# Optimization experiments

Hardware: AMD Instinct MI355X
Metric: run time of the kernel (lower is better)

Reference implementation:

```python
import jax, jax.numpy as jnp
import numpy as np

B, S, H, D = 1, 8192, 16, 128
BS = 64            # sparse_block_size
NB = S // BS       # 128 blocks
NUM_ORACLES = 32
ORACLE = S // NUM_ORACLES          # 256
LOCAL = ORACLE // BS               # 4 sliding-window blocks
PATTERN_ID = 0


def _build_block_pattern():
    """Block-level mask exactly as DKernelPredefinedSparseAttention.create_mask((0,))."""
    qb = np.arange(NB)[:, None]
    kb = np.arange(NB)[None, :]
    causal = qb >= kb
    window = (qb - kb) < LOCAL
    vert = np.zeros(NB, dtype=bool)
    real_col = int(PATTERN_ID * ORACLE + 0.5)
    vert[real_col // BS:(real_col + ORACLE) // BS] = True
    vert[0:1] = True
    mask = causal & (window | vert[None, :])
    kmax = int(mask.sum(axis=1).max())  # = 8 for this pattern
    kidx = np.zeros((NB, kmax), dtype=np.int32)
    kvalid = np.zeros((NB, kmax), dtype=bool)
    for i in range(NB):
        idx = np.nonzero(mask[i])[0]
        kidx[i, :len(idx)] = idx
        kvalid[i, :len(idx)] = True
    return kidx, kvalid


def setup_inputs() -> dict:
    key = jax.random.key(0)
    kq, kk, kv = jax.random.split(key, 3)
    q = jax.random.normal(kq, (B, S, H, D), dtype=jnp.float32)
    k = jax.random.normal(kk, (B, S, H, D), dtype=jnp.float32)
    v = jax.random.normal(kv, (B, S, H, D), dtype=jnp.float32)
    kidx_np, kvalid_np = _build_block_pattern()
    return {"q": q, "k": k, "v": v,
            "kidx": jnp.asarray(kidx_np), "kvalid": jnp.asarray(kvalid_np)}


def reference(q, k, v, kidx, kvalid):
    # q,k,v: [B,S,H,D] (bshd). kidx/kvalid: [NB, Kmax] active k-block ids per q-block.
    b, s, h, d = q.shape
    nb = s // BS
    kmax = kidx.shape[1]
    qb = q.reshape(b, nb, BS, h, d)
    kb = k.reshape(b, nb, BS, h, d)
    vb = v.reshape(b, nb, BS, h, d)
    # Gather only active k/v blocks -> [B, nb, Kmax, BS, H, D]
    kg = kb[:, kidx]
    vg = vb[:, kidx]
    scale = 1.0 / jnp.sqrt(jnp.float32(d))
    # [B, H, nb, BS(q), Kmax, BS(k)]
    scores = jnp.einsum('bqahd,bqkchd->bhqakc', qb, kg) * scale
    # element-level causal mask within the block pattern
    qpos = jnp.arange(nb)[:, None] * BS + jnp.arange(BS)[None, :]          # [nb, BS]
    kpos = kidx[..., None] * BS + jnp.arange(BS)[None, None, :]            # [nb, Kmax, BS]
    allow = (qpos[:, :, None, None] >= kpos[:, None, :, :]) & kvalid[:, None, :, None]
    scores = jnp.where(allow[None, None], scores, jnp.float32(-1e30))
    probs = jax.nn.softmax(scores.reshape(b, h, nb, BS, kmax * BS), axis=-1)
    probs = probs.reshape(scores.shape)
    out = jnp.einsum('bhqakc,bqkchd->bqahd', probs, vg)
    return out.reshape(b, s, h, d)
```

## Files before the change

kernel.cpp:

```cpp
#include <hip/hip_runtime.h>
#include <hip/hip_bf16.h>

#define HH 16
#define DD 128
#define NBQ 128
#define SS 8192

typedef __attribute__((ext_vector_type(4))) float f32x4;
typedef __attribute__((ext_vector_type(4))) short bf16x4;
typedef __attribute__((ext_vector_type(8))) short bf16x8;

__device__ __forceinline__ short f2bf_hw(float f) {
  __hip_bfloat16 b = __float2bfloat16(f);
  return __builtin_bit_cast(short, b);
}

__device__ __forceinline__ void gload_lds16(const void* g, void* l) {
  __builtin_amdgcn_global_load_lds(
      (const __attribute__((address_space(1))) void*)g,
      (__attribute__((address_space(3))) void*)l, 16, 0, 0);
}

__device__ __forceinline__ void wg_barrier() {
  asm volatile("" ::: "memory");
  __builtin_amdgcn_s_barrier();
  asm volatile("" ::: "memory");
}

__global__ __launch_bounds__(256)
void conv_fused_kernel(const float* __restrict__ kg, const float* __restrict__ vg,
                       unsigned short* __restrict__ kt2, unsigned short* __restrict__ vt3) {
  __shared__ __align__(16) unsigned short tile[128 * 72];
  const int bx  = blockIdx.x;
  const int tid = threadIdx.x;
  if (bx < 2048) {
    const int kb = bx & 127, h = bx >> 7;
    {
      const int r = tid >> 2, q = tid & 3;
      const float* vp = vg + ((size_t)(kb * 64 + r) * HH + h) * DD + q * 32;
      #pragma unroll
      for (int c = 0; c < 8; ++c) {
        f32x4 a = *(const f32x4*)(vp + c * 4);
        #pragma unroll
        for (int j = 0; j < 4; ++j)
          tile[(q * 32 + c * 4 + j) * 72 + r] = (unsigned short)f2bf_hw(a[j]);
      }
    }
    __syncthreads();
    char* obase = (char*)vt3 + (((size_t)h * NBQ + kb) << 14);
    const int l15 = tid & 15, lg = (tid >> 4) & 3;
    #pragma unroll
    for (int round = 0; round < 4; ++round) {
      const int o  = round * 4096 + tid * 16;
      const int u  = round * 4 + (tid >> 6);
      const int nd = u >> 1, hb = u & 1;
      const int d  = nd * 16 + l15;
      bf16x8 f;
      #pragma unroll
      for (int j = 0; j < 8; ++j) {
        const int key = (2 * hb + (j >> 2)) * 16 + lg * 4 + (j & 3);
        f[j] = (short)tile[d * 72 + key];
      }
      *(bf16x8*)(obase + o) = f;
    }
  } else {
    const int b2 = bx - 2048;
    const int kb = b2 & 127, h = b2 >> 7;
    {
      const int r = tid >> 2, q = tid & 3;
      const float* kp = kg + ((size_t)(kb * 64 + r) * HH + h) * DD + q * 32;
      #pragma unroll
      for (int g = 0; g < 4; ++g) {
        f32x4 a = *(const f32x4*)(kp + g * 8);
        f32x4 b = *(const f32x4*)(kp + g * 8 + 4);
        bf16x8 f;
        f[0] = f2bf_hw(a[0]); f[1] = f2bf_hw(a[1]); f[2] = f2bf_hw(a[2]); f[3] = f2bf_hw(a[3]);
        f[4] = f2bf_hw(b[0]); f[5] = f2bf_hw(b[1]); f[6] = f2bf_hw(b[2]); f[7] = f2bf_hw(b[3]);
        const int off = (((r >> 4) * 4 + q) * 64 + g * 16 + (r & 15)) * 8;
        *(bf16x8*)(&tile[off]) = f;
      }
    }
    __syncthreads();
    char* obase = (char*)kt2 + (((size_t)h * NBQ + kb) << 14);
    const char* tb = (const char*)tile;
    #pragma unroll
    for (int round = 0; round < 4; ++round) {
      const int o = round * 4096 + tid * 16;
      *(bf16x8*)(obase + o) = *(const bf16x8*)(tb + o);
    }
  }
}

__global__ __launch_bounds__(512, 4)
void sparse_attn_v24(const float* __restrict__ qg_, const unsigned short* __restrict__ kt2,
                     const unsigned short* __restrict__ vt3, float* __restrict__ outg) {
  extern __shared__ __align__(16) char lds[];

  const int bx   = blockIdx.x;
  const int w    = (bx & 7) * 128 + (bx >> 3);
  const int h    = w >> 6;
  const int qgrp = w & 63;
  const int tid  = threadIdx.x;
  const int wid  = tid >> 6;
  const int lane = tid & 63;
  const int l15  = lane & 15;
  const int lg   = lane >> 4;

  const int qlo  = qgrp * 2, qhi = qgrp * 2 + 1;
  const int qb_w = qlo + (wid >> 2);
  const int rib0 = (wid & 3) * 16;

  const int nv     = (qhi + 1 < 4) ? qhi + 1 : 4;
  const int wstart = (qlo - 3 > 4) ? qlo - 3 : 4;
  const int nw     = (qhi - wstart + 1 > 0) ? qhi - wstart + 1 : 0;
  const int nlist  = nv + nw;

  const float scale = 0.12752030522080552f;

  const int rowg = qgrp * 128 + (wid >> 2) * 64 + rib0;
  const int lb   = lane * 16;

  bf16x8 qa[4];
  {
    const float* qp = qg_ + ((size_t)(rowg + l15) * HH + h) * DD;
    #pragma unroll
    for (int kc = 0; kc < 4; ++kc) {
      const int d0 = kc * 32 + lg * 8;
      f32x4 a = *(const f32x4*)(qp + d0);
      f32x4 b = *(const f32x4*)(qp + d0 + 4);
      bf16x8 f;
      f[0] = f2bf_hw(a[0] * scale); f[1] = f2bf_hw(a[1] * scale);
      f[2] = f2bf_hw(a[2] * scale); f[3] = f2bf_hw(a[3] * scale);
      f[4] = f2bf_hw(b[0] * scale); f[5] = f2bf_hw(b[1] * scale);
      f[6] = f2bf_hw(b[2] * scale); f[7] = f2bf_hw(b[3] * scale);
      qa[kc] = f;
    }
  }

  f32x4 oa[8];
  #pragma unroll
  for (int i = 0; i < 8; ++i) oa[i] = (f32x4){0.f, 0.f, 0.f, 0.f};
  float mr = -1e30f;
  float lr = 0.f;

  const char* kbase = (const char*)kt2 + ((size_t)h * NBQ << 14);
  const char* vbase = (const char*)vt3 + ((size_t)h * NBQ << 14);
  const int o0 = wid * 1024 + lb;

  {
    #pragma unroll
    for (int p = 0; p < 2; ++p) {
      const int o = p * 8192 + o0;
      gload_lds16(kbase + o, lds + p * 8192 + wid * 1024);
    }
    #pragma unroll
    for (int p = 0; p < 2; ++p) {
      const int o = p * 8192 + o0;
      gload_lds16(vbase + o, lds + 32768 + p * 8192 + wid * 1024);
    }
  }

  for (int t = 0; t < nlist; ++t) {
    const int kb = (t < nv) ? t : (wstart + (t - nv));
    const bool valid = (kb <= qb_w) && ((qb_w - kb < 4) || (kb < 4));
    char* Kb = lds + (t & 1) * 16384;
    char* Vb = lds + 32768 + (t & 1) * 16384;
    const bool havenext = (t + 1 < nlist);

    asm volatile("s_waitcnt vmcnt(0)" ::: "memory");
    wg_barrier();

    if (havenext) {
      const int kbn = (t + 1 < nv) ? (t + 1) : (wstart + (t + 1 - nv));
      const char* ksrc = kbase + ((size_t)kbn << 14);
      const char* vsrc = vbase + ((size_t)kbn << 14);
      char* Kd = lds + ((t + 1) & 1) * 16384;
      char* Vd = lds + 32768 + ((t + 1) & 1) * 16384;
      #pragma unroll
      for (int p = 0; p < 2; ++p) {
        const int o = p * 8192 + o0;
        gload_lds16(ksrc + o, Kd + p * 8192 + wid * 1024);
      }
      #pragma unroll
      for (int p = 0; p < 2; ++p) {
        const int o = p * 8192 + o0;
        gload_lds16(vsrc + o, Vd + p * 8192 + wid * 1024);
      }
    }

    if (valid) {
      f32x4 s[4];
      #pragma unroll
      for (int kt = 0; kt < 4; ++kt) s[kt] = (f32x4){0.f, 0.f, 0.f, 0.f};
      #pragma unroll
      for (int kt = 0; kt < 4; ++kt) {
        #pragma unroll
        for (int kc = 0; kc < 4; ++kc) {
          const int off = ((kt * 4 + kc) << 10) + lb;
          bf16x8 kf = *(const bf16x8*)(Kb + off);
          s[kt] = __builtin_amdgcn_mfma_f32_16x16x32_bf16(kf, qa[kc], s[kt], 0, 0, 0);
        }
      }

      if (kb == qb_w) {
        const int rib = rib0 + l15;
        #pragma unroll
        for (int kt = 0; kt < 4; ++kt)
          #pragma unroll
          for (int r = 0; r < 4; ++r) {
            const int key = kt * 16 + lg * 4 + r;
            if (rib < key) s[kt][r] = -1e30f;
          }
      }

      {
        float m01 = fmaxf(fmaxf(s[0][0], s[0][1]), fmaxf(fmaxf(s[0][2], s[0][3]), s[1][0]));
        float m02 = fmaxf(fmaxf(s[1][1], s[1][2]), fmaxf(fmaxf(s[1][3], s[2][0]), s[2][1]));
        float m03 = fmaxf(fmaxf(s[2][2], s[2][3]), fmaxf(fmaxf(s[3][0], s[3][1]), s[3][2]));
        float lanemax = fmaxf(fmaxf(m01, m02), fmaxf(m03, s[3][3]));
        if (!__all(lanemax <= mr + 8.f)) {
          float mx = lanemax;
          mx = fmaxf(mx, __shfl_xor(mx, 16));
          mx = fmaxf(mx, __shfl_xor(mx, 32));
          const float mnew = fmaxf(mr, mx);
          const float sc = __builtin_amdgcn_exp2f(mr - mnew);
          lr *= sc;
          mr = mnew;
          const float s0 = __shfl(sc, lg * 4 + 0);
          const float s1 = __shfl(sc, lg * 4 + 1);
          const float s2 = __shfl(sc, lg * 4 + 2);
          const float s3 = __shfl(sc, lg * 4 + 3);
          #pragma unroll
          for (int nd = 0; nd < 8; ++nd) {
            oa[nd][0] *= s0; oa[nd][1] *= s1;
            oa[nd][2] *= s2; oa[nd][3] *= s3;
          }
        }
        float lsum = 0.f;
        #pragma unroll
        for (int kt = 0; kt < 4; ++kt)
          #pragma unroll
          for (int r = 0; r < 4; ++r) {
            const float p = __builtin_amdgcn_exp2f(s[kt][r] - mr);
            s[kt][r] = p;
            lsum += p;
          }
        lr += lsum;
      }

      bf16x4 pa[4];
      #pragma unroll
      for (int kt = 0; kt < 4; ++kt) {
        unsigned u0 = (unsigned)(unsigned short)f2bf_hw(s[kt][0]) |
                      ((unsigned)(unsigned short)f2bf_hw(s[kt][1]) << 16);
        unsigned u1 = (unsigned)(unsigned short)f2bf_hw(s[kt][2]) |
                      ((unsigned)(unsigned short)f2bf_hw(s[kt][3]) << 16);
        uint2 uu; uu.x = u0; uu.y = u1;
        pa[kt] = __builtin_bit_cast(bf16x4, uu);
      }

      #pragma unroll
      for (int nd = 0; nd < 8; ++nd) {
        #pragma unroll
        for (int hb = 0; hb < 2; ++hb) {
          const int off = ((nd * 2 + hb) << 10) + lb;
          bf16x8 v2 = *(const bf16x8*)(Vb + off);
          bf16x4 vlo = __builtin_shufflevector(v2, v2, 0, 1, 2, 3);
          bf16x4 vhi = __builtin_shufflevector(v2, v2, 4, 5, 6, 7);
          oa[nd] = __builtin_amdgcn_mfma_f32_16x16x16bf16_1k(pa[2 * hb],     vlo, oa[nd], 0, 0, 0);
          oa[nd] = __builtin_amdgcn_mfma_f32_16x16x16bf16_1k(pa[2 * hb + 1], vhi, oa[nd], 0, 0, 0);
        }
      }
    }
  }

  {
    float l = lr;
    l += __shfl_xor(l, 16);
    l += __shfl_xor(l, 32);
    const float inv = 1.0f / l;
    const float i0 = __shfl(inv, lg * 4 + 0);
    const float i1 = __shfl(inv, lg * 4 + 1);
    const float i2 = __shfl(inv, lg * 4 + 2);
    const float i3 = __shfl(inv, lg * 4 + 3);
    float* op = outg + ((size_t)rowg * HH + h) * DD;
    #pragma unroll
    for (int nd = 0; nd < 8; ++nd) {
      const int d = nd * 16 + l15;
      op[(size_t)(lg * 4 + 0) * HH * DD + d] = oa[nd][0] * i0;
      op[(size_t)(lg * 4 + 1) * HH * DD + d] = oa[nd][1] * i1;
      op[(size_t)(lg * 4 + 2) * HH * DD + d] = oa[nd][2] * i2;
      op[(size_t)(lg * 4 + 3) * HH * DD + d] = oa[nd][3] * i3;
    }
  }
}

extern "C" void kernel_launch(void* const* d_in, const int* in_sizes, int n_in,
                              void* d_out, int out_size, void* d_ws, size_t ws_size,
                              hipStream_t stream) {
  const float* q = (const float*)d_in[0];
  const float* k = (const float*)d_in[1];
  const float* v = (const float*)d_in[2];
  float* out = (float*)d_out;
  const size_t elems = (size_t)HH * SS * DD;
  unsigned short* kt2 = (unsigned short*)d_ws;
  unsigned short* vt3 = kt2 + elems;

  conv_fused_kernel<<<4096, 256, 0, stream>>>(k, v, kt2, vt3);
  sparse_attn_v24<<<dim3(NBQ / 2 * HH), 512, 65536, stream>>>(q, kt2, vt3, out);
}
```

Measured before the change: 95.60 us.

## Software-pipeline PV matmul one iteration behind QK with triple-buffered V

Defers the P·V MFMA of each key block to the next loop iteration, so it can overlap with the next block's QK^T and softmax work. V gets a triple-buffered LDS ring so the deferred block's V is not overwritten by the prefetch, which raises dynamic LDS from 64KB to 80KB. Launch bounds drop from 4 to 2 waves-per-EU to leave room for the extra live registers. The cost is lower occupancy and higher register pressure.

```diff
diff --git a/kernel.cpp b/kernel.cpp
--- a/kernel.cpp
+++ b/kernel.cpp
@@ -91,8 +91,8 @@
   }
 }
 
-__global__ __launch_bounds__(512, 4)
-void sparse_attn_v24(const float* __restrict__ qg_, const unsigned short* __restrict__ kt2,
+__global__ __launch_bounds__(512, 2)
+void sparse_attn_v25(const float* __restrict__ qg_, const unsigned short* __restrict__ kt2,
                      const unsigned short* __restrict__ vt3, float* __restrict__ outg) {
   extern __shared__ __align__(16) char lds[];
 
@@ -143,6 +143,10 @@
   float mr = -1e30f;
   float lr = 0.f;
 
+  bf16x4 pa_prev[4];
+  bool   pvalid = false;
+  int    vprev  = 0;
+
   const char* kbase = (const char*)kt2 + ((size_t)h * NBQ << 14);
   const char* vbase = (const char*)vt3 + ((size_t)h * NBQ << 14);
   const int o0 = wid * 1024 + lb;
@@ -164,7 +168,7 @@
     const int kb = (t < nv) ? t : (wstart + (t - nv));
     const bool valid = (kb <= qb_w) && ((qb_w - kb < 4) || (kb < 4));
     char* Kb = lds + (t & 1) * 16384;
-    char* Vb = lds + 32768 + (t & 1) * 16384;
+    const int vcur = t % 3;
     const bool havenext = (t + 1 < nlist);
 
     asm volatile("s_waitcnt vmcnt(0)" ::: "memory");
@@ -175,7 +179,7 @@
       const char* ksrc = kbase + ((size_t)kbn << 14);
       const char* vsrc = vbase + ((size_t)kbn << 14);
       char* Kd = lds + ((t + 1) & 1) * 16384;
-      char* Vd = lds + 32768 + ((t + 1) & 1) * 16384;
+      char* Vd = lds + 32768 + ((t + 1) % 3) * 16384;
       #pragma unroll
       for (int p = 0; p < 2; ++p) {
         const int o = p * 8192 + o0;
@@ -188,8 +192,8 @@
       }
     }
 
+    f32x4 s[4];
     if (valid) {
-      f32x4 s[4];
       #pragma unroll
       for (int kt = 0; kt < 4; ++kt) s[kt] = (f32x4){0.f, 0.f, 0.f, 0.f};
       #pragma unroll
@@ -201,7 +205,25 @@
           s[kt] = __builtin_amdgcn_mfma_f32_16x16x32_bf16(kf, qa[kc], s[kt], 0, 0, 0);
         }
       }
-
+    }
+
+    if (pvalid) {
+      char* Vp = lds + 32768 + vprev * 16384;
+      #pragma unroll
+      for (int nd = 0; nd < 8; ++nd) {
+        #pragma unroll
+        for (int hb = 0; hb < 2; ++hb) {
+          const int off = ((nd * 2 + hb) << 10) + lb;
+          bf16x8 v2 = *(const bf16x8*)(Vp + off);
+          bf16x4 vlo = __builtin_shufflevector(v2, v2, 0, 1, 2, 3);
+          bf16x4 vhi = __builtin_shufflevector(v2, v2, 4, 5, 6, 7);
+          oa[nd] = __builtin_amdgcn_mfma_f32_16x16x16bf16_1k(pa_prev[2 * hb],     vlo, oa[nd], 0, 0, 0);
+          oa[nd] = __builtin_amdgcn_mfma_f32_16x16x16bf16_1k(pa_prev[2 * hb + 1], vhi, oa[nd], 0, 0, 0);
+        }
+      }
+    }
+
+    if (valid) {
       if (kb == qb_w) {
         const int rib = rib0 + l15;
         #pragma unroll
@@ -248,7 +270,6 @@
         lr += lsum;
       }
 
-      bf16x4 pa[4];
       #pragma unroll
       for (int kt = 0; kt < 4; ++kt) {
         unsigned u0 = (unsigned)(unsigned short)f2bf_hw(s[kt][0]) |
@@ -256,20 +277,27 @@
         unsigned u1 = (unsigned)(unsigned short)f2bf_hw(s[kt][2]) |
                       ((unsigned)(unsigned short)f2bf_hw(s[kt][3]) << 16);
         uint2 uu; uu.x = u0; uu.y = u1;
-        pa[kt] = __builtin_bit_cast(bf16x4, uu);
-      }
-
-      #pragma unroll
-      for (int nd = 0; nd < 8; ++nd) {
-        #pragma unroll
-        for (int hb = 0; hb < 2; ++hb) {
-          const int off = ((nd * 2 + hb) << 10) + lb;
-          bf16x8 v2 = *(const bf16x8*)(Vb + off);
-          bf16x4 vlo = __builtin_shufflevector(v2, v2, 0, 1, 2, 3);
-          bf16x4 vhi = __builtin_shufflevector(v2, v2, 4, 5, 6, 7);
-          oa[nd] = __builtin_amdgcn_mfma_f32_16x16x16bf16_1k(pa[2 * hb],     vlo, oa[nd], 0, 0, 0);
-          oa[nd] = __builtin_amdgcn_mfma_f32_16x16x16bf16_1k(pa[2 * hb + 1], vhi, oa[nd], 0, 0, 0);
-        }
+        pa_prev[kt] = __builtin_bit_cast(bf16x4, uu);
+      }
+      pvalid = true;
+      vprev  = vcur;
+    } else {
+      pvalid = false;
+    }
+  }
+
+  if (pvalid) {
+    char* Vp = lds + 32768 + vprev * 16384;
+    #pragma unroll
+    for (int nd = 0; nd < 8; ++nd) {
+      #pragma unroll
+      for (int hb = 0; hb < 2; ++hb) {
+        const int off = ((nd * 2 + hb) << 10) + lb;
+        bf16x8 v2 = *(const bf16x8*)(Vp + off);
+        bf16x4 vlo = __builtin_shufflevector(v2, v2, 0, 1, 2, 3);
+        bf16x4 vhi = __builtin_shufflevector(v2, v2, 4, 5, 6, 7);
+        oa[nd] = __builtin_amdgcn_mfma_f32_16x16x16bf16_1k(pa_prev[2 * hb],     vlo, oa[nd], 0, 0, 0);
+        oa[nd] = __builtin_amdgcn_mfma_f32_16x16x16bf16_1k(pa_prev[2 * hb + 1], vhi, oa[nd], 0, 0, 0);
       }
     }
   }
@@ -307,5 +335,5 @@
   unsigned short* vt3 = kt2 + elems;
 
   conv_fused_kernel<<<4096, 256, 0, stream>>>(k, v, kt2, vt3);
-  sparse_attn_v24<<<dim3(NBQ / 2 * HH), 512, 65536, stream>>>(q, kt2, vt3, out);
-}
+  sparse_attn_v25<<<dim3(NBQ / 2 * HH), 512, 81920, stream>>>(q, kt2, vt3, out);
+}
```

Result: no change. 95.61 us (+0.0%).
